# Optimization experiments

Measured on AMD Instinct MI355X. Metric: run time of the kernel, lower is better.

## Reference

```python
import jax, jax.numpy as jnp
import numpy as np

N_GRAPHS = 1250
NEG_SLOPE = 0.2

def gat_layer(x, src, dst, W, a_src, a_dst, b, concat):
    # x: [N, Fin]; W: [Fin, H*C]; a_src/a_dst: [H, C]; b: [H*C] or [C]
    N = x.shape[0]
    H, C = a_src.shape
    h = (x @ W).reshape(N, H, C)                      # [N,H,C]
    alpha_s = jnp.sum(h * a_src[None], axis=-1)       # [N,H]
    alpha_d = jnp.sum(h * a_dst[None], axis=-1)       # [N,H]
    e = jax.nn.leaky_relu(alpha_s[src] + alpha_d[dst], NEG_SLOPE)  # [E,H]
    # segment softmax over incoming edges of each target node
    m = jax.ops.segment_max(e, dst, num_segments=N)   # [N,H]
    m = jnp.where(jnp.isfinite(m), m, 0.0)
    ex = jnp.exp(e - m[dst])
    s = jax.ops.segment_sum(ex, dst, num_segments=N)  # [N,H]
    alpha = ex / (s[dst] + 1e-16)                     # [E,H]
    msg = h[src] * alpha[..., None]                   # [E,H,C]
    out = jax.ops.segment_sum(msg, dst, num_segments=N)  # [N,H,C]
    out = out.reshape(N, H * C) if concat else out.mean(axis=1)
    return out + b

def setup_inputs() -> dict:
    key = jax.random.key(0)
    ks = jax.random.split(key, 13)
    N, E = 50000, 100000
    x = jax.random.normal(ks[0], (N, 78), dtype=jnp.float32)
    edge_index = jax.random.randint(ks[1], (2, E), 0, N, dtype=jnp.int64)
    # sorted segment ids -> every graph non-empty (~40 nodes each)
    batch = jnp.sort(jax.random.randint(ks[2], (N,), 0, N_GRAPHS, dtype=jnp.int64))
    g = lambda k, shape, fan: jax.random.normal(k, shape, dtype=jnp.float32) / np.float32(np.sqrt(fan))
    return {
        'x': x, 'edge_index': edge_index, 'batch': batch,
        'W1': g(ks[3], (78, 780), 78), 'a_src1': g(ks[4], (10, 78), 78), 'a_dst1': g(ks[5], (10, 78), 78),
        'b1': jnp.zeros((780,), jnp.float32),
        'W2': g(ks[6], (780, 128), 780), 'a_src2': g(ks[7], (1, 128), 128), 'a_dst2': g(ks[8], (1, 128), 128),
        'b2': jnp.zeros((128,), jnp.float32),
        'fc_w': g(ks[9], (128, 128), 128), 'fc_b': jnp.zeros((128,), jnp.float32),
    }

def reference(x, edge_index, batch, W1, a_src1, a_dst1, b1, W2, a_src2, a_dst2, b2, fc_w, fc_b):
    N = x.shape[0]
    loop = jnp.arange(N, dtype=edge_index.dtype)
    src = jnp.concatenate([edge_index[0], loop])  # add self loops (PyG default)
    dst = jnp.concatenate([edge_index[1], loop])
    # dropout layers are identity in eval mode
    h = jax.nn.elu(gat_layer(x, src, dst, W1, a_src1, a_dst1, b1, concat=True))   # [N,780]
    h = jax.nn.relu(gat_layer(h, src, dst, W2, a_src2, a_dst2, b2, concat=True))  # [N,128]
    g = jax.ops.segment_max(h, batch, num_segments=N_GRAPHS)                      # [G,128]
    g = jnp.where(jnp.isfinite(g), g, 0.0)
    return jax.nn.relu(g @ fc_w + fc_b)
```

## Files before the change

kernel.cpp:

```cpp
#include <hip/hip_runtime.h>
#include <hip/hip_bf16.h>
#include <cstdint>

#define CAP 32
typedef __hip_bfloat16 bf16;
typedef __attribute__((ext_vector_type(8))) short short8;
typedef __attribute__((ext_vector_type(4))) float f32x4;

__device__ __forceinline__ float sb2f(short s) {
  unsigned int u = ((unsigned int)(unsigned short)s) << 16;
  return __uint_as_float(u);
}
__device__ __forceinline__ short f2sb(float f) {
  bf16 h = __float2bfloat16(f);
  return *reinterpret_cast<short*>(&h);
}


__global__ void k_detect(const int* __restrict__ ei, int* __restrict__ flag) {
  __shared__ int any;
  if (threadIdx.x == 0) any = 0;
  __syncthreads();
  int v = 0;
  for (int i = 1 + 2 * threadIdx.x; i < 2000; i += 512) v |= ei[i];
  if (v) atomicOr(&any, 1);
  __syncthreads();
  if (threadIdx.x == 0) flag[0] = (any == 0) ? 1 : 0;
}

__device__ __forceinline__ void edge_sd(const int* __restrict__ ei, int e, int f,
                                        int& src, int& dst) {
  if (e < 100000) {
    if (f) { src = ei[2 * e]; dst = ei[200000 + 2 * e]; }
    else   { src = ei[e];     dst = ei[100000 + e]; }
  } else { src = dst = e - 100000; }
  src = min(max(src, 0), 49999);
  dst = min(max(dst, 0), 49999);
}

__global__ void k_prep(const float* __restrict__ x, const float* __restrict__ W1,
                       const float* __restrict__ W2, const float* __restrict__ aw1,
                       const float* __restrict__ dw1, bf16* __restrict__ xb,
                       bf16* __restrict__ W1t, bf16* __restrict__ W2t,
                       bf16* __restrict__ Wat, float* __restrict__ zp, int zeroWords) {
  int i = blockIdx.x * 256 + threadIdx.x;
  if (i < zeroWords) zp[i] = 0.f;
  const int n_xb = 50000 * 96;
  const int n_w1 = 832 * 96;
  const int n_w2 = 128 * 832;
  const int n_wa = 32 * 96;
  if (i < n_xb) {
    int r = i / 96, k = i - r * 96;
    xb[i] = __float2bfloat16(k < 78 ? x[r * 78 + k] : 0.f);
  } else if (i < n_xb + n_w1) {
    int jdx = i - n_xb;
    int np = jdx / 96, k = jdx - np * 96;
    int h = np / 80, j = np - h * 80;
    float v = 0.f;
    if (k < 78 && np < 800 && j < 78) v = W1[k * 780 + (h * 78 + j)];
    W1t[jdx] = __float2bfloat16(v);
  } else if (i < n_xb + n_w1 + n_w2) {
    int jdx = i - n_xb - n_w1;
    int c = jdx / 832, kp = jdx - c * 832;
    int h = kp / 80, j = kp - h * 80;
    float v = 0.f;
    if (kp < 800 && j < 78) v = W2[(h * 78 + j) * 128 + c];
    W2t[jdx] = __float2bfloat16(v);
  } else if (i < n_xb + n_w1 + n_w2 + n_wa) {
    int jdx = i - n_xb - n_w1 - n_w2;
    int c = jdx / 96, k = jdx - c * 96;
    float s = 0.f;
    if (k < 78 && c < 20) {
      const float* w = (c < 10) ? aw1 : dw1;
      int h = (c < 10) ? c : c - 10;
      const float* wrow = W1 + k * 780 + h * 78;
      const float* arow = w + h * 78;
      for (int q = 0; q < 78; q++) s += wrow[q] * arow[q];
    }
    Wat[c * 96 + k] = __float2bfloat16(s);
  }
}

__global__ __launch_bounds__(256) void k_gemm1(const bf16* __restrict__ xb,
                                               const bf16* __restrict__ W1t,
                                               const bf16* __restrict__ Wat,
                                               const float* __restrict__ b1,
                                               bf16* __restrict__ H1,
                                               float* __restrict__ as1,
                                               float* __restrict__ ad1) {
  __shared__ __align__(16) short Als[64 * 104];
  __shared__ __align__(16) short Bls[64 * 104];
  __shared__ __align__(16) short Wls[32 * 104];
  __shared__ __align__(16) float Cls[64 * 68];
  __shared__ float b1s[832];
  const int t = threadIdx.x;
  const int w = t >> 6, l = t & 63, l15 = l & 15, q = l >> 4;
  const int rowBase = blockIdx.x * 64;
  for (int s = t; s < 768; s += 256) {
    int row = s / 12, kg = s - row * 12;
    short8 v = {};
    int gr = rowBase + row;
    if (gr < 50000) v = *(const short8*)((const short*)xb + (size_t)gr * 96 + kg * 8);
    *(short8*)&Als[row * 104 + kg * 8] = v;
  }
  for (int s = t; s < 384; s += 256) {
    int row = s / 12, kg = s - row * 12;
    *(short8*)&Wls[row * 104 + kg * 8] =
        *(const short8*)((const short*)Wat + (size_t)row * 96 + kg * 8);
  }
  for (int s = t; s < 832; s += 256) {
    int h = s / 80, j = s - h * 80;
    b1s[s] = (s < 800 && j < 78) ? b1[h * 78 + j] : 0.f;
  }
  short8 breg[3];
  int bn[3], bk[3];
#pragma unroll
  for (int i = 0; i < 3; i++) {
    int s = t + i * 256;
    bn[i] = s / 12; bk[i] = s - bn[i] * 12;
    breg[i] = *(const short8*)((const short*)W1t + (size_t)bn[i] * 96 + bk[i] * 8);
  }
  for (int cc = 0; cc < 13; cc++) {
    __syncthreads();
#pragma unroll
    for (int i = 0; i < 3; i++) *(short8*)&Bls[bn[i] * 104 + bk[i] * 8] = breg[i];
    if (cc < 12) {
#pragma unroll
      for (int i = 0; i < 3; i++)
        breg[i] = *(const short8*)((const short*)W1t +
                                   (size_t)((cc + 1) * 64 + bn[i]) * 96 + bk[i] * 8);
    }
    __syncthreads();
    f32x4 acc[4] = {};
#pragma unroll
    for (int ks = 0; ks < 3; ks++) {
      short8 a = *(const short8*)&Als[(w * 16 + l15) * 104 + ks * 32 + q * 8];
#pragma unroll
      for (int nt = 0; nt < 4; nt++) {
        short8 b = *(const short8*)&Bls[(nt * 16 + l15) * 104 + ks * 32 + q * 8];
        acc[nt] = __builtin_amdgcn_mfma_f32_16x16x32_bf16(a, b, acc[nt], 0, 0, 0);
      }
    }
    __syncthreads();
#pragma unroll
    for (int nt = 0; nt < 4; nt++)
#pragma unroll
      for (int r = 0; r < 4; r++)
        Cls[(w * 16 + q * 4 + r) * 68 + nt * 16 + l15] = acc[nt][r];
    __syncthreads();
    {
      int r = t >> 2, c0 = (t & 3) * 16;
      int gr = rowBase + r;
      if (gr < 50000) {
        short8 o0, o1;
#pragma unroll
        for (int c = 0; c < 8; c++) o0[c] = f2sb(Cls[r * 68 + c0 + c] + b1s[cc * 64 + c0 + c]);
#pragma unroll
        for (int c = 0; c < 8; c++) o1[c] = f2sb(Cls[r * 68 + c0 + 8 + c] + b1s[cc * 64 + c0 + 8 + c]);
        short* dst = (short*)H1 + (size_t)gr * 832 + cc * 64 + c0;
        *(short8*)dst = o0;
        *(short8*)(dst + 8) = o1;
      }
    }
  }
  f32x4 acc2[2] = {};
#pragma unroll
  for (int ks = 0; ks < 3; ks++) {
    short8 a = *(const short8*)&Als[(w * 16 + l15) * 104 + ks * 32 + q * 8];
#pragma unroll
    for (int nt = 0; nt < 2; nt++) {
      short8 b = *(const short8*)&Wls[(nt * 16 + l15) * 104 + ks * 32 + q * 8];
      acc2[nt] = __builtin_amdgcn_mfma_f32_16x16x32_bf16(a, b, acc2[nt], 0, 0, 0);
    }
  }
  const int gr0 = rowBase + w * 16 + q * 4;
#pragma unroll
  for (int nt = 0; nt < 2; nt++) {
    int c = nt * 16 + l15;
#pragma unroll
    for (int r = 0; r < 4; r++) {
      int gr = gr0 + r;
      if (gr < 50000) {
        if (c < 10)       as1[gr * 10 + c] = acc2[nt][r];
        else if (c < 20)  ad1[gr * 10 + (c - 10)] = acc2[nt][r];
      }
    }
  }
}

__global__ void k_scatter(const int* __restrict__ ei, const int* __restrict__ flag,
                          int* __restrict__ cnt, int* __restrict__ csr) {
  int e = blockIdx.x * 256 + threadIdx.x;
  if (e >= 150000) return;
  int f = flag[0], src, dst;
  edge_sd(ei, e, f, src, dst);
  int pos = atomicAdd(&cnt[dst], 1);
  if (pos < CAP) csr[dst * CAP + pos] = src;
}

__global__ __launch_bounds__(256) void k_agg1(const bf16* __restrict__ H1,
                                              const float* __restrict__ as1,
                                              const float* __restrict__ ad1,
                                              const int* __restrict__ csr,
                                              const int* __restrict__ cnt,
                                              bf16* __restrict__ HL2) {
  __shared__ float sexw[2][CAP * 10];
  __shared__ float sden[2][16];
  __shared__ int ssrc[2][CAP];
  __shared__ int scnt[2];
  const int t = threadIdx.x;
  const int sub = t >> 7, tt = t & 127;
  const int n = blockIdx.x * 2 + sub;
  if (t < 2) scnt[t] = min(cnt[blockIdx.x * 2 + t], CAP);
  if (t >= 32 && t < 64) { int z = t - 32; sden[z >> 4][z & 15] = 0.f; }
  __syncthreads();
  const int cn = scnt[sub];
  if (tt < cn) ssrc[sub][tt] = csr[n * CAP + tt];
  __syncthreads();
  for (int wv = tt; wv < cn * 10; wv += 128) {
    int k = wv / 10, h = wv - k * 10;
    int src = ssrc[sub][k];
    float e = as1[src * 10 + h] + ad1[n * 10 + h];
    e = e >= 0.f ? e : 0.2f * e;
    float ex = __expf(e);
    sexw[sub][wv] = ex;
    atomicAdd(&sden[sub][h], ex);
  }
  __syncthreads();
  if (tt < 100) {
    const int head = tt / 10;
    const int j0 = tt * 8;
    float acc[8] = {};
    const float* sw = sexw[sub] + head;
    const short* H1s = (const short*)H1;
    for (int k = 0; k < cn; k++) {
      int src = ssrc[sub][k];
      short8 hv = *(const short8*)(H1s + (size_t)src * 832 + j0);
      float wk = sw[k * 10];
#pragma unroll
      for (int c = 0; c < 8; c++) acc[c] += wk * sb2f(hv[c]);
    }
    const float r0 = 1.f / (sden[sub][head] + 1e-16f);
    short8 ov;
#pragma unroll
    for (int c = 0; c < 8; c++) {
      float v = acc[c] * r0;
      v = v > 0.f ? v : __expf(v) - 1.f;
      ov[c] = f2sb(v);
    }
    *(short8*)((short*)HL2 + (size_t)n * 832 + j0) = ov;
  } else if (tt < 104) {
    short8 z = {};
    *(short8*)((short*)HL2 + (size_t)n * 832 + tt * 8) = z;
  }
}

__global__ __launch_bounds__(256) void k_gemm2(const bf16* __restrict__ A,
                                               const bf16* __restrict__ W2t,
                                               const float* __restrict__ AW2,
                                               const float* __restrict__ DW2,
                                               bf16* __restrict__ H2,
                                               float* __restrict__ as2,
                                               float* __restrict__ ad2) {
  __shared__ __align__(16) short Als[64 * 72];
  __shared__ __align__(16) short Bls[128 * 72];
  __shared__ float sAW[128], sDW[128];
  __shared__ float sS[4][64], sD[4][64];
  const int t = threadIdx.x;
  const int w = t >> 6, l = t & 63, l15 = l & 15, q = l >> 4;
  const int rowBase = blockIdx.x * 64;
  if (t < 128) sAW[t] = AW2[t];
  else         sDW[t - 128] = DW2[t - 128];
  const int ar = t >> 2, ak = t & 3;
  short8 areg[2], breg[4];
  {
    int gr0 = rowBase + ar;
#pragma unroll
    for (int i = 0; i < 2; i++) {
      short8 v = {};
      int gr = gr0;
      if (gr < 50000)
        v = *(const short8*)((const short*)A + (size_t)gr * 832 + 0 + (ak * 2 + i) * 8);
      areg[i] = v;
    }
#pragma unroll
    for (int i = 0; i < 4; i++) {
      int s = t + i * 256;
      int col = s >> 3, kg = s & 7;
      breg[i] = *(const short8*)((const short*)W2t + (size_t)col * 832 + 0 + kg * 8);
    }
  }
  f32x4 acc[4][2] = {};
  for (int kb = 0; kb < 832; kb += 64) {
    __syncthreads();
#pragma unroll
    for (int i = 0; i < 2; i++)
      *(short8*)&Als[ar * 72 + (ak * 2 + i) * 8] = areg[i];
#pragma unroll
    for (int i = 0; i < 4; i++) {
      int s = t + i * 256;
      int col = s >> 3, kg = s & 7;
      *(short8*)&Bls[col * 72 + kg * 8] = breg[i];
    }
    if (kb < 768) {
      int kn = kb + 64;
      int gr = rowBase + ar;
#pragma unroll
      for (int i = 0; i < 2; i++) {
        short8 v = {};
        if (gr < 50000)
          v = *(const short8*)((const short*)A + (size_t)gr * 832 + kn + (ak * 2 + i) * 8);
        areg[i] = v;
      }
#pragma unroll
      for (int i = 0; i < 4; i++) {
        int s = t + i * 256;
        int col = s >> 3, kg = s & 7;
        breg[i] = *(const short8*)((const short*)W2t + (size_t)col * 832 + kn + kg * 8);
      }
    }
    __syncthreads();
#pragma unroll
    for (int ks = 0; ks < 2; ks++) {
      short8 a[4];
#pragma unroll
      for (int mt = 0; mt < 4; mt++)
        a[mt] = *(const short8*)&Als[(mt * 16 + l15) * 72 + ks * 32 + q * 8];
#pragma unroll
      for (int ntl = 0; ntl < 2; ntl++) {
        short8 b = *(const short8*)&Bls[((w * 2 + ntl) * 16 + l15) * 72 + ks * 32 + q * 8];
#pragma unroll
        for (int mt = 0; mt < 4; mt++)
          acc[mt][ntl] = __builtin_amdgcn_mfma_f32_16x16x32_bf16(a[mt], b, acc[mt][ntl], 0, 0, 0);
      }
    }
  }
  const int col0 = w * 32 + l15, col1 = col0 + 16;
  const float aw0 = sAW[col0], aw1 = sAW[col1];
  const float dw0 = sDW[col0], dw1 = sDW[col1];
  f32x4 sp[4], dp[4];
#pragma unroll
  for (int mt = 0; mt < 4; mt++) {
    sp[mt] = acc[mt][0] * aw0 + acc[mt][1] * aw1;
    dp[mt] = acc[mt][0] * dw0 + acc[mt][1] * dw1;
  }
#pragma unroll
  for (int m = 1; m < 16; m <<= 1) {
#pragma unroll
    for (int mt = 0; mt < 4; mt++)
#pragma unroll
      for (int r = 0; r < 4; r++) {
        sp[mt][r] += __shfl_xor(sp[mt][r], m, 64);
        dp[mt][r] += __shfl_xor(dp[mt][r], m, 64);
      }
  }
  if (l15 == 0) {
#pragma unroll
    for (int mt = 0; mt < 4; mt++)
#pragma unroll
      for (int r = 0; r < 4; r++) {
        sS[w][mt * 16 + q * 4 + r] = sp[mt][r];
        sD[w][mt * 16 + q * 4 + r] = dp[mt][r];
      }
  }
#pragma unroll
  for (int mt = 0; mt < 4; mt++) {
    int gr0 = rowBase + mt * 16 + q * 4;
#pragma unroll
    for (int ntl = 0; ntl < 2; ntl++) {
      int gc = w * 32 + ntl * 16 + l15;
#pragma unroll
      for (int r = 0; r < 4; r++) {
        int gr = gr0 + r;
        if (gr < 50000) H2[(size_t)gr * 128 + gc] = __float2bfloat16(acc[mt][ntl][r]);
      }
    }
  }
  __syncthreads();
  if (t < 64) {
    int gr = rowBase + t;
    if (gr < 50000) as2[gr] = sS[0][t] + sS[1][t] + sS[2][t] + sS[3][t];
  } else if (t < 128) {
    int r2 = t - 64;
    int gr = rowBase + r2;
    if (gr < 50000) ad2[gr] = sD[0][r2] + sD[1][r2] + sD[2][r2] + sD[3][r2];
  }
}

__global__ __launch_bounds__(128) void k_agg2(const bf16* __restrict__ H2,
                                              const float* __restrict__ as2,
                                              const float* __restrict__ ad2,
                                              const int* __restrict__ csr,
                                              const int* __restrict__ cnt,
                                              const float* __restrict__ b2,
                                              const int* __restrict__ batch,
                                              const int* __restrict__ flag,
                                              float* __restrict__ g) {
  __shared__ int ssrc[CAP];
  __shared__ float sexw[CAP];
  __shared__ float sden;
  __shared__ int scnt, sbv;
  const int t = threadIdx.x;
  const int n = blockIdx.x;
  if (t == 0) {
    scnt = min(cnt[n], CAP);
    sden = 0.f;
    int b = flag[0] ? batch[2 * n] : batch[n];
    sbv = min(max(b, 0), 1249);
  }
  __syncthreads();
  const int cn = scnt;
  if (t < cn) {
    int src = csr[n * CAP + t];
    ssrc[t] = src;
    float e = as2[src] + ad2[n];
    e = e >= 0.f ? e : 0.2f * e;
    float ex = __expf(e);
    sexw[t] = ex;
    atomicAdd(&sden, ex);
  }
  __syncthreads();
  const short* H2s = (const short*)H2;
  float acc = 0.f;
  if (cn > 0) {
    short hv = H2s[(size_t)ssrc[0] * 128 + t];
    for (int k = 0; k < cn; k++) {
      short hn = hv;
      if (k + 1 < cn) hn = H2s[(size_t)ssrc[k + 1] * 128 + t];
      acc += sexw[k] * sb2f(hv);
      hv = hn;
    }
  }
  float v = acc / (sden + 1e-16f) + b2[t];
  v = v > 0.f ? v : 0.f;
  atomicMax((int*)&g[sbv * 128 + t], __float_as_int(v));
}

__global__ __launch_bounds__(128) void k_fc(const float* __restrict__ g,
                                            const float* __restrict__ fw,
                                            const float* __restrict__ fb,
                                            float* __restrict__ out) {
  const int n = blockIdx.x, t = threadIdx.x;
  __shared__ float grow[128];
  grow[t] = g[n * 128 + t];
  __syncthreads();
  float acc = fb[t];
  for (int k = 0; k < 128; k++) acc += grow[k] * fw[k * 128 + t];
  out[n * 128 + t] = acc > 0.f ? acc : 0.f;
}

extern "C" void kernel_launch(void* const* d_in, const int* in_sizes, int n_in,
                              void* d_out, int out_size, void* d_ws, size_t ws_size,
                              hipStream_t stream) {
  const float* x     = (const float*)d_in[0];
  const int*   ei    = (const int*)d_in[1];
  const int*   batch = (const int*)d_in[2];
  const float* W1    = (const float*)d_in[3];
  const float* as1w  = (const float*)d_in[4];
  const float* ad1w  = (const float*)d_in[5];
  const float* b1    = (const float*)d_in[6];
  const float* W2    = (const float*)d_in[7];
  const float* as2w  = (const float*)d_in[8];
  const float* ad2w  = (const float*)d_in[9];
  const float* b2    = (const float*)d_in[10];
  const float* fcw   = (const float*)d_in[11];
  const float* fcb   = (const float*)d_in[12];
  float* out = (float*)d_out;

  char* p = (char*)d_ws;
  size_t off = 0;
  auto alloc = [&](size_t bytes) -> void* {
    void* r = p + off;
    off = (off + bytes + 15) & ~(size_t)15;
    return r;
  };
  int*   cnt = (int*)  alloc(50000 * 4);
  float* g   = (float*)alloc(160000 * 4);
  size_t zeroWords = off / 4;
  float* as1 = (float*)alloc(500000 * 4);
  float* ad1 = (float*)alloc(500000 * 4);
  float* as2 = (float*)alloc(50000 * 4);
  float* ad2 = (float*)alloc(50000 * 4);
  bf16*  W1t = (bf16*) alloc((size_t)832 * 96 * 2);
  bf16*  W2t = (bf16*) alloc((size_t)128 * 832 * 2);
  bf16*  Wat = (bf16*) alloc((size_t)32 * 96 * 2);
  bf16*  h1  = (bf16*) alloc((size_t)50000 * 832 * 2);
  bf16*  hl2 = (bf16*) alloc((size_t)50000 * 832 * 2);
  int*   csr = (int*)  alloc((size_t)50000 * CAP * 4);
  void*  uni = alloc((size_t)50000 * 128 * 2);
  bf16*  xb  = (bf16*)uni;
  bf16*  h2  = (bf16*)uni;
  int*   flag = (int*) alloc(16);
  (void)ws_size; (void)in_sizes; (void)n_in; (void)out_size;

  k_detect<<<1, 256, 0, stream>>>(ei, flag);
  int prepN = 50000 * 96 + 832 * 96 + 128 * 832 + 32 * 96;
  k_prep<<<(prepN + 255) / 256, 256, 0, stream>>>(
      x, W1, W2, as1w, ad1w, xb, W1t, W2t, Wat, (float*)d_ws, (int)zeroWords);

  k_gemm1<<<782, 256, 0, stream>>>(xb, W1t, Wat, b1, h1, as1, ad1);
  k_scatter<<<(150000 + 255) / 256, 256, 0, stream>>>(ei, flag, cnt, csr);
  k_agg1<<<25000, 256, 0, stream>>>(h1, as1, ad1, csr, cnt, hl2);
  k_gemm2<<<782, 256, 0, stream>>>(hl2, W2t, as2w, ad2w, h2, as2, ad2);
  k_agg2<<<50000, 128, 0, stream>>>(h2, as2, ad2, csr, cnt, b2, batch, flag, g);
  k_fc<<<1250, 128, 0, stream>>>(g, fcw, fcb, out);
}
```

Measured before the change: 278.7 us.

## Fuse layer-2 aggregation, graph max-pool and FC into one per-graph kernel

Graph start offsets are computed from the sorted batch vector inside the scatter kernel. A new per-graph kernel then runs the layer-2 attention aggregation for all nodes of a graph, keeps a running column max in registers, and applies the final FC+ReLU. This replaces the per-node agg2 kernel with its global atomicMax and the separate FC kernel, which removes 50000 small blocks, the atomics and one launch. The cost is that only 1250 blocks remain, with serial per-node loops and no prefetch, so the GPU may be underused and latency-bound.

```diff
diff --git a/kernel.cpp b/kernel.cpp
--- a/kernel.cpp
+++ b/kernel.cpp
@@ -189,13 +189,28 @@
 }
 
 __global__ void k_scatter(const int* __restrict__ ei, const int* __restrict__ flag,
-                          int* __restrict__ cnt, int* __restrict__ csr) {
+                          int* __restrict__ cnt, int* __restrict__ csr,
+                          const int* __restrict__ batch, int* __restrict__ gstart) {
   int e = blockIdx.x * 256 + threadIdx.x;
   if (e >= 150000) return;
   int f = flag[0], src, dst;
   edge_sd(ei, e, f, src, dst);
   int pos = atomicAdd(&cnt[dst], 1);
   if (pos < CAP) csr[dst * CAP + pos] = src;
+  if (e < 50000) {
+    int b1 = f ? batch[2 * e] : batch[e];
+    b1 = min(max(b1, 0), 1249);
+    int b0 = -1;
+    if (e > 0) {
+      b0 = f ? batch[2 * (e - 1)] : batch[e - 1];
+      b0 = min(max(b0, 0), 1249);
+    }
+    for (int gg = b0 + 1; gg <= b1; gg++) gstart[gg] = e;
+    if (e == 0) gstart[1250] = 50000;
+    if (e == 49999) {
+      for (int gg = b1 + 1; gg <= 1249; gg++) gstart[gg] = 50000;
+    }
+  }
 }
 
 __global__ __launch_bounds__(256) void k_agg1(const bf16* __restrict__ H1,
@@ -387,66 +402,73 @@
   }
 }
 
-__global__ __launch_bounds__(128) void k_agg2(const bf16* __restrict__ H2,
+__global__ __launch_bounds__(128) void k_pool(const bf16* __restrict__ H2,
                                               const float* __restrict__ as2,
                                               const float* __restrict__ ad2,
                                               const int* __restrict__ csr,
                                               const int* __restrict__ cnt,
                                               const float* __restrict__ b2,
-                                              const int* __restrict__ batch,
-                                              const int* __restrict__ flag,
-                                              float* __restrict__ g) {
-  __shared__ int ssrc[CAP];
-  __shared__ float sexw[CAP];
-  __shared__ float sden;
-  __shared__ int scnt, sbv;
+                                              const int* __restrict__ gstart,
+                                              const float* __restrict__ fw,
+                                              const float* __restrict__ fb,
+                                              float* __restrict__ out) {
+  __shared__ int ssrc[8][CAP];
+  __shared__ float sw[8][CAP];
+  __shared__ float sden[8];
+  __shared__ int scn[8];
+  __shared__ float grow[128];
   const int t = threadIdx.x;
-  const int n = blockIdx.x;
-  if (t == 0) {
-    scnt = min(cnt[n], CAP);
-    sden = 0.f;
-    int b = flag[0] ? batch[2 * n] : batch[n];
-    sbv = min(max(b, 0), 1249);
-  }
-  __syncthreads();
-  const int cn = scnt;
-  if (t < cn) {
-    int src = csr[n * CAP + t];
-    ssrc[t] = src;
-    float e = as2[src] + ad2[n];
-    e = e >= 0.f ? e : 0.2f * e;
-    float ex = __expf(e);
-    sexw[t] = ex;
-    atomicAdd(&sden, ex);
-  }
-  __syncthreads();
+  const int gid = blockIdx.x;
+  const int ns = gstart[gid], ne = gstart[gid + 1];
+  const float bt = b2[t];
+  float mcol = 0.f;
   const short* H2s = (const short*)H2;
-  float acc = 0.f;
-  if (cn > 0) {
-    short hv = H2s[(size_t)ssrc[0] * 128 + t];
-    for (int k = 0; k < cn; k++) {
-      short hn = hv;
-      if (k + 1 < cn) hn = H2s[(size_t)ssrc[k + 1] * 128 + t];
-      acc += sexw[k] * sb2f(hv);
-      hv = hn;
-    }
-  }
-  float v = acc / (sden + 1e-16f) + b2[t];
-  v = v > 0.f ? v : 0.f;
-  atomicMax((int*)&g[sbv * 128 + t], __float_as_int(v));
-}
-
-__global__ __launch_bounds__(128) void k_fc(const float* __restrict__ g,
-                                            const float* __restrict__ fw,
-                                            const float* __restrict__ fb,
-                                            float* __restrict__ out) {
-  const int n = blockIdx.x, t = threadIdx.x;
-  __shared__ float grow[128];
-  grow[t] = g[n * 128 + t];
-  __syncthreads();
-  float acc = fb[t];
-  for (int k = 0; k < 128; k++) acc += grow[k] * fw[k * 128 + t];
-  out[n * 128 + t] = acc > 0.f ? acc : 0.f;
+  for (int base = ns; base < ne; base += 8) {
+    if (t < 8) {
+      sden[t] = 0.f;
+      scn[t] = (base + t < ne) ? min(cnt[base + t], CAP) : 0;
+    }
+    __syncthreads();
+    {
+      const int ng = t >> 4, s = t & 15;
+      int n = base + ng;
+      if (n < ne) {
+        int cn = scn[ng];
+        float ad = ad2[n];
+#pragma unroll
+        for (int r = 0; r < 2; r++) {
+          int k = s + r * 16;
+          if (k < cn) {
+            int src = csr[n * CAP + k];
+            ssrc[ng][k] = src;
+            float e = as2[src] + ad;
+            e = e >= 0.f ? e : 0.2f * e;
+            float ex = __expf(e);
+            sw[ng][k] = ex;
+            atomicAdd(&sden[ng], ex);
+          }
+        }
+      }
+    }
+    __syncthreads();
+#pragma unroll
+    for (int g8 = 0; g8 < 8; g8++) {
+      int n = base + g8;
+      if (n >= ne) break;
+      int cn = scn[g8];
+      float acc = 0.f;
+      for (int k = 0; k < cn; k++)
+        acc += sw[g8][k] * sb2f(H2s[(size_t)ssrc[g8][k] * 128 + t]);
+      float v = acc / (sden[g8] + 1e-16f) + bt;
+      mcol = fmaxf(mcol, v > 0.f ? v : 0.f);
+    }
+    __syncthreads();
+  }
+  grow[t] = mcol;
+  __syncthreads();
+  float accf = fb[t];
+  for (int k = 0; k < 128; k++) accf += grow[k] * fw[k * 128 + t];
+  out[gid * 128 + t] = accf > 0.f ? accf : 0.f;
 }
 
 extern "C" void kernel_launch(void* const* d_in, const int* in_sizes, int n_in,
@@ -475,7 +497,6 @@
     return r;
   };
   int*   cnt = (int*)  alloc(50000 * 4);
-  float* g   = (float*)alloc(160000 * 4);
   size_t zeroWords = off / 4;
   float* as1 = (float*)alloc(500000 * 4);
   float* ad1 = (float*)alloc(500000 * 4);
@@ -487,6 +508,7 @@
   bf16*  h1  = (bf16*) alloc((size_t)50000 * 832 * 2);
   bf16*  hl2 = (bf16*) alloc((size_t)50000 * 832 * 2);
   int*   csr = (int*)  alloc((size_t)50000 * CAP * 4);
+  int*   gstart = (int*)alloc(1251 * 4);
   void*  uni = alloc((size_t)50000 * 128 * 2);
   bf16*  xb  = (bf16*)uni;
   bf16*  h2  = (bf16*)uni;
@@ -499,9 +521,8 @@
       x, W1, W2, as1w, ad1w, xb, W1t, W2t, Wat, (float*)d_ws, (int)zeroWords);
 
   k_gemm1<<<782, 256, 0, stream>>>(xb, W1t, Wat, b1, h1, as1, ad1);
-  k_scatter<<<(150000 + 255) / 256, 256, 0, stream>>>(ei, flag, cnt, csr);
+  k_scatter<<<(150000 + 255) / 256, 256, 0, stream>>>(ei, flag, cnt, csr, batch, gstart);
   k_agg1<<<25000, 256, 0, stream>>>(h1, as1, ad1, csr, cnt, hl2);
   k_gemm2<<<782, 256, 0, stream>>>(hl2, W2t, as2w, ad2w, h2, as2, ad2);
-  k_agg2<<<50000, 128, 0, stream>>>(h2, as2, ad2, csr, cnt, b2, batch, flag, g);
-  k_fc<<<1250, 128, 0, stream>>>(g, fcw, fcb, out);
-}
+  k_pool<<<1250, 128, 0, stream>>>(h2, as2, ad2, csr, cnt, b2, gstart, fcw, fcb, out);
+}
```

After: 306.1 us. +9.8%, slower.

## Aggregate layer-1 inputs before projection to shrink gathered feature width

Applied to the files above, without the earlier changes.

Layer 1 now gathers the 96-wide input features per head using the attention weights, producing a per-node Z of 10 heads x 96 values. A new GEMM then projects each head's aggregate with that head's slice of W1 and applies bias and ELU. This uses linearity of attention aggregation so the gather reads 96-wide rows instead of 832-wide projected rows, and the 50000x832 H1 intermediate is never written. In exchange it writes and reads a 960-wide Z buffer, adds one kernel launch, and the second GEMM reloads its weights for every head without prefetch.

```diff
diff --git a/kernel.cpp b/kernel.cpp
--- a/kernel.cpp
+++ b/kernel.cpp
@@ -81,18 +81,12 @@
   }
 }
 
-__global__ __launch_bounds__(256) void k_gemm1(const bf16* __restrict__ xb,
-                                               const bf16* __restrict__ W1t,
+__global__ __launch_bounds__(256) void k_alpha(const bf16* __restrict__ xb,
                                                const bf16* __restrict__ Wat,
-                                               const float* __restrict__ b1,
-                                               bf16* __restrict__ H1,
                                                float* __restrict__ as1,
                                                float* __restrict__ ad1) {
   __shared__ __align__(16) short Als[64 * 104];
-  __shared__ __align__(16) short Bls[64 * 104];
   __shared__ __align__(16) short Wls[32 * 104];
-  __shared__ __align__(16) float Cls[64 * 68];
-  __shared__ float b1s[832];
   const int t = threadIdx.x;
   const int w = t >> 6, l = t & 63, l15 = l & 15, q = l >> 4;
   const int rowBase = blockIdx.x * 64;
@@ -108,61 +102,7 @@
     *(short8*)&Wls[row * 104 + kg * 8] =
         *(const short8*)((const short*)Wat + (size_t)row * 96 + kg * 8);
   }
-  for (int s = t; s < 832; s += 256) {
-    int h = s / 80, j = s - h * 80;
-    b1s[s] = (s < 800 && j < 78) ? b1[h * 78 + j] : 0.f;
-  }
-  short8 breg[3];
-  int bn[3], bk[3];
-#pragma unroll
-  for (int i = 0; i < 3; i++) {
-    int s = t + i * 256;
-    bn[i] = s / 12; bk[i] = s - bn[i] * 12;
-    breg[i] = *(const short8*)((const short*)W1t + (size_t)bn[i] * 96 + bk[i] * 8);
-  }
-  for (int cc = 0; cc < 13; cc++) {
-    __syncthreads();
-#pragma unroll
-    for (int i = 0; i < 3; i++) *(short8*)&Bls[bn[i] * 104 + bk[i] * 8] = breg[i];
-    if (cc < 12) {
-#pragma unroll
-      for (int i = 0; i < 3; i++)
-        breg[i] = *(const short8*)((const short*)W1t +
-                                   (size_t)((cc + 1) * 64 + bn[i]) * 96 + bk[i] * 8);
-    }
-    __syncthreads();
-    f32x4 acc[4] = {};
-#pragma unroll
-    for (int ks = 0; ks < 3; ks++) {
-      short8 a = *(const short8*)&Als[(w * 16 + l15) * 104 + ks * 32 + q * 8];
-#pragma unroll
-      for (int nt = 0; nt < 4; nt++) {
-        short8 b = *(const short8*)&Bls[(nt * 16 + l15) * 104 + ks * 32 + q * 8];
-        acc[nt] = __builtin_amdgcn_mfma_f32_16x16x32_bf16(a, b, acc[nt], 0, 0, 0);
-      }
-    }
-    __syncthreads();
-#pragma unroll
-    for (int nt = 0; nt < 4; nt++)
-#pragma unroll
-      for (int r = 0; r < 4; r++)
-        Cls[(w * 16 + q * 4 + r) * 68 + nt * 16 + l15] = acc[nt][r];
-    __syncthreads();
-    {
-      int r = t >> 2, c0 = (t & 3) * 16;
-      int gr = rowBase + r;
-      if (gr < 50000) {
-        short8 o0, o1;
-#pragma unroll
-        for (int c = 0; c < 8; c++) o0[c] = f2sb(Cls[r * 68 + c0 + c] + b1s[cc * 64 + c0 + c]);
-#pragma unroll
-        for (int c = 0; c < 8; c++) o1[c] = f2sb(Cls[r * 68 + c0 + 8 + c] + b1s[cc * 64 + c0 + 8 + c]);
-        short* dst = (short*)H1 + (size_t)gr * 832 + cc * 64 + c0;
-        *(short8*)dst = o0;
-        *(short8*)(dst + 8) = o1;
-      }
-    }
-  }
+  __syncthreads();
   f32x4 acc2[2] = {};
 #pragma unroll
   for (int ks = 0; ks < 3; ks++) {
@@ -198,12 +138,12 @@
   if (pos < CAP) csr[dst * CAP + pos] = src;
 }
 
-__global__ __launch_bounds__(256) void k_agg1(const bf16* __restrict__ H1,
+__global__ __launch_bounds__(256) void k_zagg(const bf16* __restrict__ xb,
                                               const float* __restrict__ as1,
                                               const float* __restrict__ ad1,
                                               const int* __restrict__ csr,
                                               const int* __restrict__ cnt,
-                                              bf16* __restrict__ HL2) {
+                                              bf16* __restrict__ Z) {
   __shared__ float sexw[2][CAP * 10];
   __shared__ float sden[2][16];
   __shared__ int ssrc[2][CAP];
@@ -227,15 +167,15 @@
     atomicAdd(&sden[sub][h], ex);
   }
   __syncthreads();
-  if (tt < 100) {
-    const int head = tt / 10;
-    const int j0 = tt * 8;
+  if (tt < 120) {
+    const int head = tt / 12;
+    const int j0 = (tt - head * 12) * 8;
     float acc[8] = {};
     const float* sw = sexw[sub] + head;
-    const short* H1s = (const short*)H1;
+    const short* xs = (const short*)xb;
     for (int k = 0; k < cn; k++) {
       int src = ssrc[sub][k];
-      short8 hv = *(const short8*)(H1s + (size_t)src * 832 + j0);
+      short8 hv = *(const short8*)(xs + (size_t)src * 96 + j0);
       float wk = sw[k * 10];
 #pragma unroll
       for (int c = 0; c < 8; c++) acc[c] += wk * sb2f(hv[c]);
@@ -243,15 +183,72 @@
     const float r0 = 1.f / (sden[sub][head] + 1e-16f);
     short8 ov;
 #pragma unroll
-    for (int c = 0; c < 8; c++) {
-      float v = acc[c] * r0;
-      v = v > 0.f ? v : __expf(v) - 1.f;
-      ov[c] = f2sb(v);
-    }
-    *(short8*)((short*)HL2 + (size_t)n * 832 + j0) = ov;
-  } else if (tt < 104) {
-    short8 z = {};
-    *(short8*)((short*)HL2 + (size_t)n * 832 + tt * 8) = z;
+    for (int c = 0; c < 8; c++) ov[c] = f2sb(acc[c] * r0);
+    *(short8*)((short*)Z + (size_t)n * 960 + head * 96 + j0) = ov;
+  }
+}
+
+__global__ __launch_bounds__(256) void k_gemm1b(const bf16* __restrict__ Z,
+                                                const bf16* __restrict__ W1t,
+                                                const float* __restrict__ b1,
+                                                bf16* __restrict__ HL2) {
+  __shared__ __align__(16) short Als[64 * 104];
+  __shared__ __align__(16) short Bls[80 * 104];
+  __shared__ __align__(16) float Cls[64 * 84];
+  __shared__ float b1s[832];
+  const int t = threadIdx.x;
+  const int w = t >> 6, l = t & 63, l15 = l & 15, q = l >> 4;
+  const int rowBase = blockIdx.x * 64;
+  for (int s = t; s < 832; s += 256) {
+    int h = s / 80, j = s - h * 80;
+    b1s[s] = (s < 800 && j < 78) ? b1[h * 78 + j] : 0.f;
+  }
+  for (int h = 0; h < 10; h++) {
+    __syncthreads();
+    for (int s = t; s < 768; s += 256) {
+      int row = s / 12, kg = s - row * 12;
+      short8 v = {};
+      int gr = rowBase + row;
+      if (gr < 50000)
+        v = *(const short8*)((const short*)Z + (size_t)gr * 960 + h * 96 + kg * 8);
+      *(short8*)&Als[row * 104 + kg * 8] = v;
+    }
+    for (int s = t; s < 960; s += 256) {
+      int row = s / 12, kg = s - row * 12;
+      *(short8*)&Bls[row * 104 + kg * 8] =
+          *(const short8*)((const short*)W1t + (size_t)(h * 80 + row) * 96 + kg * 8);
+    }
+    __syncthreads();
+    f32x4 acc[5] = {};
+#pragma unroll
+    for (int ks = 0; ks < 3; ks++) {
+      short8 a = *(const short8*)&Als[(w * 16 + l15) * 104 + ks * 32 + q * 8];
+#pragma unroll
+      for (int nt = 0; nt < 5; nt++) {
+        short8 b = *(const short8*)&Bls[(nt * 16 + l15) * 104 + ks * 32 + q * 8];
+        acc[nt] = __builtin_amdgcn_mfma_f32_16x16x32_bf16(a, b, acc[nt], 0, 0, 0);
+      }
+    }
+#pragma unroll
+    for (int nt = 0; nt < 5; nt++)
+#pragma unroll
+      for (int r = 0; r < 4; r++)
+        Cls[(w * 16 + q * 4 + r) * 84 + nt * 16 + l15] = acc[nt][r];
+    __syncthreads();
+    for (int s = t; s < 640; s += 256) {
+      int row = s / 10, grp = s - row * 10;
+      int gr = rowBase + row;
+      if (gr < 50000) {
+        short8 ov;
+#pragma unroll
+        for (int c = 0; c < 8; c++) {
+          float v = Cls[row * 84 + grp * 8 + c] + b1s[h * 80 + grp * 8 + c];
+          v = v > 0.f ? v : __expf(v) - 1.f;
+          ov[c] = f2sb(v);
+        }
+        *(short8*)((short*)HL2 + (size_t)gr * 832 + h * 80 + grp * 8) = ov;
+      }
+    }
   }
 }
 
@@ -484,11 +481,11 @@
   bf16*  W1t = (bf16*) alloc((size_t)832 * 96 * 2);
   bf16*  W2t = (bf16*) alloc((size_t)128 * 832 * 2);
   bf16*  Wat = (bf16*) alloc((size_t)32 * 96 * 2);
-  bf16*  h1  = (bf16*) alloc((size_t)50000 * 832 * 2);
+  bf16*  xb  = (bf16*) alloc((size_t)50000 * 96 * 2);
   bf16*  hl2 = (bf16*) alloc((size_t)50000 * 832 * 2);
   int*   csr = (int*)  alloc((size_t)50000 * CAP * 4);
-  void*  uni = alloc((size_t)50000 * 128 * 2);
-  bf16*  xb  = (bf16*)uni;
+  void*  uni = alloc((size_t)50000 * 960 * 2);
+  bf16*  z   = (bf16*)uni;
   bf16*  h2  = (bf16*)uni;
   int*   flag = (int*) alloc(16);
   (void)ws_size; (void)in_sizes; (void)n_in; (void)out_size;
@@ -498,9 +495,10 @@
   k_prep<<<(prepN + 255) / 256, 256, 0, stream>>>(
       x, W1, W2, as1w, ad1w, xb, W1t, W2t, Wat, (float*)d_ws, (int)zeroWords);
 
-  k_gemm1<<<782, 256, 0, stream>>>(xb, W1t, Wat, b1, h1, as1, ad1);
+  k_alpha<<<782, 256, 0, stream>>>(xb, Wat, as1, ad1);
   k_scatter<<<(150000 + 255) / 256, 256, 0, stream>>>(ei, flag, cnt, csr);
-  k_agg1<<<25000, 256, 0, stream>>>(h1, as1, ad1, csr, cnt, hl2);
+  k_zagg<<<25000, 256, 0, stream>>>(xb, as1, ad1, csr, cnt, z);
+  k_gemm1b<<<782, 256, 0, stream>>>(z, W1t, b1, hl2);
   k_gemm2<<<782, 256, 0, stream>>>(hl2, W2t, as2w, ad2w, h2, as2, ad2);
   k_agg2<<<50000, 128, 0, stream>>>(h2, as2, ad2, csr, cnt, b2, batch, flag, g);
   k_fc<<<1250, 128, 0, stream>>>(g, fcw, fcb, out);
```

New measurement: 316.8 us. 1.14x slower.
